# Kernel tuning notes

Hardware: AMD Instinct MI355X
Metric: run time of the kernel (lower is better)

## Reference

```python
import jax, jax.numpy as jnp
import numpy as np

B, T, C = 8, 1024, 512
H = 8
E = C // 2  # split_idx == per-head dim e


def setup_inputs() -> dict:
    key = jax.random.key(0)
    ks = jax.random.split(key, 6)
    s = 0.02
    return {
        "x": jax.random.normal(ks[0], (B, T, C), dtype=jnp.float32),
        "Wq": jax.random.normal(ks[1], (E * H, E), dtype=jnp.float32) * s,
        "Wk": jax.random.normal(ks[2], (E * H, E), dtype=jnp.float32) * s,
        "Wv": jax.random.normal(ks[3], (E * H, E), dtype=jnp.float32) * s,
        "Wu": jax.random.normal(ks[4], (C - E, E * H), dtype=jnp.float32) * s,
        "bu": jnp.zeros((C - E,), dtype=jnp.float32),
    }


def reference(x, Wq, Wk, Wv, Wu, bu):
    # coupling split: x1 drives attention, x2 gets additive update
    x1 = x[..., :E]           # [B,T,E]
    x2 = x[..., E:]           # [B,T,C-E]
    scale = E ** (-0.25)
    # torch Linear: y = x W^T ; output viewed as (heads, e) -> heads-major rows
    q = jnp.einsum('bti,oi->bto', x1, Wq).reshape(B, T, H, E) * scale
    k = jnp.einsum('bti,oi->bto', x1, Wk).reshape(B, T, H, E) * scale
    v = jnp.einsum('bti,oi->bto', x1, Wv).reshape(B, T, H, E)
    # attention scores [B,H,T,T]
    dot = jnp.einsum('bthe,bshe->bhts', q, k)
    attn = jax.nn.softmax(dot, axis=-1)
    out = jnp.einsum('bhts,bshe->bthe', attn, v).reshape(B, T, H * E)
    unified = jnp.einsum('bto,co->btc', out, Wu) + bu  # [B,T,C-E]
    return jnp.concatenate([x1, x2 + unified], axis=-1)
```

## Files before the change

kernel.cpp:

```cpp
#include <hip/hip_runtime.h>
#include <hip/hip_bf16.h>

#define BB 8
#define TT 1024
#define CC 512
#define HH 8
#define EE 256
#define MM (BB*TT)
#define HE (HH*EE)

using short8 = __attribute__((ext_vector_type(8))) short;
using f32x16 = __attribute__((ext_vector_type(16))) float;
using uint2v = __attribute__((ext_vector_type(2))) unsigned int;

__device__ __forceinline__ float bf2f(unsigned short u) {
  union { float f; unsigned int i; } v; v.i = ((unsigned int)u) << 16; return v.f;
}
__device__ __forceinline__ unsigned short f2bf(float f) {
  union { float f; unsigned int i; } v; v.f = f;
  unsigned int r = v.i + 0x7FFFu + ((v.i >> 16) & 1u);
  return (unsigned short)(r >> 16);
}
__device__ __forceinline__ unsigned int pk_bf16(float lo, float hi) {
  unsigned int r;
  asm("v_cvt_pk_bf16_f32 %0, %1, %2" : "=v"(r) : "v"(lo), "v"(hi));
  return r;
}
__device__ __forceinline__ void gll16(const void* g, void* l) {
  __builtin_amdgcn_global_load_lds(
      (const __attribute__((address_space(1))) unsigned int*)g,
      (__attribute__((address_space(3))) unsigned int*)l, 16, 0, 0);
}

#define FSTR 72
__global__ __launch_bounds__(512) void qkv_fused_kernel(const float* __restrict__ x,
                                                        const float* __restrict__ Wq,
                                                        const float* __restrict__ Wk,
                                                        const float* __restrict__ Wv,
                                                        unsigned short* __restrict__ outq,
                                                        unsigned short* __restrict__ outk,
                                                        unsigned short* __restrict__ outvt,
                                                        float* __restrict__ out) {
  __shared__ unsigned short smem[4 * 128 * FSTR];
  unsigned short* As = smem;
  unsigned short* Bs[3] = { smem + 128 * FSTR, smem + 2 * 128 * FSTR, smem + 3 * 128 * FSTR };

  const int tid = threadIdx.x;
  const int lane = tid & 63;
  const int wid = tid >> 6;
  const int wr = wid >> 2, wc = wid & 3;
  const int lo = lane & 31, hi = lane >> 5;

  int bid = blockIdx.x;
  int r = bid >> 3;
  int mt = (bid & 7) * 8 + (r & 7);
  int nt = r >> 3;
  const int m0 = mt * 128;
  const int n0 = nt * 128;

  const float* Wp[3] = { Wq, Wk, Wv };
  const float scl[3] = { 0.25f * 1.44269504089f, 0.25f, 1.0f };

  const int srow = tid >> 2;
  const int sc0 = (tid & 3) * 16;

  float4 ra[4], rb[3][4];
  f32x16 acc[3][2];
#pragma unroll
  for (int w = 0; w < 3; ++w)
#pragma unroll
    for (int mi = 0; mi < 2; ++mi)
#pragma unroll
      for (int q = 0; q < 16; ++q) acc[w][mi][q] = 0.f;

#pragma unroll
  for (int j = 0; j < 4; ++j)
    ra[j] = *reinterpret_cast<const float4*>(&x[(size_t)(m0 + srow) * CC + sc0 + 4 * j]);
#pragma unroll
  for (int w = 0; w < 3; ++w)
#pragma unroll
    for (int j = 0; j < 4; ++j)
      rb[w][j] = *reinterpret_cast<const float4*>(&Wp[w][(size_t)(n0 + srow) * EE + sc0 + 4 * j]);

  for (int t = 0; t < 4; ++t) {
    {
      union { unsigned int u[4]; short8 v; } p0, p1;
      p0.u[0] = pk_bf16(ra[0].x, ra[0].y); p0.u[1] = pk_bf16(ra[0].z, ra[0].w);
      p0.u[2] = pk_bf16(ra[1].x, ra[1].y); p0.u[3] = pk_bf16(ra[1].z, ra[1].w);
      p1.u[0] = pk_bf16(ra[2].x, ra[2].y); p1.u[1] = pk_bf16(ra[2].z, ra[2].w);
      p1.u[2] = pk_bf16(ra[3].x, ra[3].y); p1.u[3] = pk_bf16(ra[3].z, ra[3].w);
      *reinterpret_cast<short8*>(&As[srow * FSTR + sc0]) = p0.v;
      *reinterpret_cast<short8*>(&As[srow * FSTR + sc0 + 8]) = p1.v;
#pragma unroll
      for (int w = 0; w < 3; ++w) {
        union { unsigned int u[4]; short8 v; } q0, q1;
        q0.u[0] = pk_bf16(rb[w][0].x, rb[w][0].y); q0.u[1] = pk_bf16(rb[w][0].z, rb[w][0].w);
        q0.u[2] = pk_bf16(rb[w][1].x, rb[w][1].y); q0.u[3] = pk_bf16(rb[w][1].z, rb[w][1].w);
        q1.u[0] = pk_bf16(rb[w][2].x, rb[w][2].y); q1.u[1] = pk_bf16(rb[w][2].z, rb[w][2].w);
        q1.u[2] = pk_bf16(rb[w][3].x, rb[w][3].y); q1.u[3] = pk_bf16(rb[w][3].z, rb[w][3].w);
        *reinterpret_cast<short8*>(&Bs[w][srow * FSTR + sc0]) = q0.v;
        *reinterpret_cast<short8*>(&Bs[w][srow * FSTR + sc0 + 8]) = q1.v;
      }
    }
    if (n0 == 0) {
      int k0 = t * 64;
#pragma unroll
      for (int j = 0; j < 4; ++j)
        *reinterpret_cast<float4*>(&out[(size_t)(m0 + srow) * CC + k0 + sc0 + 4 * j]) = ra[j];
    }
    asm volatile("s_waitcnt lgkmcnt(0)" ::: "memory");
    __builtin_amdgcn_s_barrier();
    __builtin_amdgcn_sched_barrier(0);

    if (t + 1 < 4) {
      int k0 = (t + 1) * 64;
#pragma unroll
      for (int j = 0; j < 4; ++j)
        ra[j] = *reinterpret_cast<const float4*>(&x[(size_t)(m0 + srow) * CC + k0 + sc0 + 4 * j]);
#pragma unroll
      for (int w = 0; w < 3; ++w)
#pragma unroll
        for (int j = 0; j < 4; ++j)
          rb[w][j] = *reinterpret_cast<const float4*>(&Wp[w][(size_t)(n0 + srow) * EE + k0 + sc0 + 4 * j]);
    }

    __builtin_amdgcn_s_setprio(1);
#pragma unroll
    for (int ks = 0; ks < 4; ++ks) {
      short8 af[2];
#pragma unroll
      for (int mi = 0; mi < 2; ++mi)
        af[mi] = *reinterpret_cast<const short8*>(&As[(64 * wr + 32 * mi + lo) * FSTR + ks * 16 + hi * 8]);
#pragma unroll
      for (int w = 0; w < 3; ++w) {
        short8 bf = *reinterpret_cast<const short8*>(&Bs[w][(32 * wc + lo) * FSTR + ks * 16 + hi * 8]);
#pragma unroll
        for (int mi = 0; mi < 2; ++mi)
          acc[w][mi] = __builtin_amdgcn_mfma_f32_32x32x16_bf16(af[mi], bf, acc[w][mi], 0, 0, 0);
      }
    }
    __builtin_amdgcn_s_setprio(0);
    __builtin_amdgcn_s_barrier();
    __builtin_amdgcn_sched_barrier(0);
  }

#pragma unroll
  for (int w = 0; w < 2; ++w) {
    unsigned short* op = (w == 0) ? outq : outk;
#pragma unroll
    for (int mi = 0; mi < 2; ++mi) {
#pragma unroll
      for (int q = 0; q < 16; ++q) {
        int rr = (q & 3) + 8 * (q >> 2) + 4 * hi;
        int m = m0 + 64 * wr + 32 * mi + rr;
        int n = n0 + 32 * wc + lo;
        op[(size_t)m * HE + n] = f2bf(acc[w][mi][q] * scl[w]);
      }
    }
  }

  unsigned short* Tr = smem;
  __syncthreads();
#pragma unroll
  for (int mi = 0; mi < 2; ++mi)
#pragma unroll
    for (int q = 0; q < 16; ++q) {
      int rr = (q & 3) + 8 * (q >> 2) + 4 * hi;
      Tr[(32 * wc + lo) * 136 + 64 * wr + 32 * mi + rr] = f2bf(acc[2][mi][q]);
    }
  __syncthreads();
  {
    const int b = m0 >> 10;
    const int t0m = m0 & 1023;
#pragma unroll
    for (int p = 0; p < 4; ++p) {
      int nr = p * 32 + (tid >> 4);
      int chunk = tid & 15;
      int n = n0 + nr;
      size_t drow = ((size_t)b * 8 + (n >> 8)) * 256 + (n & 255);
      *reinterpret_cast<short8*>(&outvt[drow * TT + t0m + chunk * 8]) =
          *reinterpret_cast<const short8*>(&Tr[nr * 136 + chunk * 8]);
    }
  }
}

#define SBLK 32
__global__ __launch_bounds__(256, 2) void attn_kernel(const unsigned short* __restrict__ qg,
                                                      const unsigned short* __restrict__ kg,
                                                      const unsigned short* __restrict__ vtg,
                                                      unsigned short* __restrict__ og) {
  __shared__ char smem[66048];
  unsigned short* Kbuf = (unsigned short*)smem;
  unsigned short* Vbuf = (unsigned short*)(smem + 32768);
  float* lpart = (float*)(smem + 65536);

  const int tid = threadIdx.x;
  const int lane = tid & 63;
  const int wid = tid >> 6;
  const int lo = lane & 31, hi = lane >> 5;

  int logical = (blockIdx.x & 7) * 64 + (blockIdx.x >> 3);
  const int bh = logical >> 3;
  const int t0 = (logical & 7) * 128;
  const int b = bh >> 3, h = bh & 7;
  const size_t qkbase = (size_t)b * TT * HE + (size_t)h * EE;
  const size_t vtbase = (size_t)bh * EE * TT;
  const unsigned short* kg_base = kg + qkbase;
  const unsigned short* vt_base = vtg + vtbase;

  short8 qf[16];
  {
    const unsigned short* qrow = qg + qkbase + (size_t)(t0 + 32 * wid + lo) * HE + hi * 8;
#pragma unroll
    for (int ks = 0; ks < 16; ++ks)
      qf[ks] = *reinterpret_cast<const short8*>(qrow + ks * 16);
  }

  f32x16 Oacc[8];
#pragma unroll
  for (int et = 0; et < 8; ++et)
#pragma unroll
    for (int q = 0; q < 16; ++q) Oacc[et][q] = 0.f;
  float lacc = 0.f;

  const int k_sub = lane >> 5;
  const int k_g   = lane & 31;
  const int v_er  = lane >> 2;
  const int v_g   = lane & 3;
  const int v_gs  = v_g ^ ((lane >> 3) & 3);

#define STAGE_TILE(TIDX, BUF)                                                        \
  {                                                                                  \
    const unsigned short* kt = kg_base + (size_t)(TIDX) * SBLK * HE;                 \
    const unsigned short* vt = vt_base + (size_t)(TIDX) * SBLK;                      \
    unsigned short* Kb = Kbuf + (BUF) * (SBLK * 256);                                \
    unsigned short* Vb = Vbuf + (BUF) * (256 * SBLK);                                \
    _Pragma("unroll")                                                                \
    for (int i = 0; i < 4; ++i) {                                                    \
      int row = 8 * wid + 2 * i + k_sub;                                             \
      int gs = k_g ^ (row & 7);                                                      \
      gll16(kt + (size_t)row * HE + gs * 8, Kb + (8 * wid + 2 * i) * 256);           \
    }                                                                                \
    _Pragma("unroll")                                                                \
    for (int i = 0; i < 4; ++i) {                                                    \
      int row = 64 * wid + 16 * i + v_er;                                            \
      gll16(vt + (size_t)row * TT + v_gs * 8, Vb + (64 * wid + 16 * i) * SBLK);      \
    }                                                                                \
  }

  STAGE_TILE(0, 0)
  asm volatile("s_waitcnt vmcnt(0)" ::: "memory");
  __builtin_amdgcn_s_barrier();
  __builtin_amdgcn_sched_barrier(0);

  for (int t = 0; t < 32; ++t) {
    const int cur = t & 1;
    if (t + 1 < 32) STAGE_TILE(t + 1, cur ^ 1)

    const unsigned short* Kb = Kbuf + cur * (SBLK * 256);
    const unsigned short* Vb = Vbuf + cur * (256 * SBLK);

    f32x16 sacc;
#pragma unroll
    for (int q = 0; q < 16; ++q) sacc[q] = 0.f;
    const int sxor = lo & 7;
#pragma unroll
    for (int ks = 0; ks < 16; ++ks) {
      int slot = (ks * 2 + hi) ^ sxor;
      short8 kf = *reinterpret_cast<const short8*>(&Kb[lo * 256 + slot * 8]);
      sacc = __builtin_amdgcn_mfma_f32_32x32x16_bf16(kf, qf[ks], sacc, 0, 0, 0);
    }

    short8 pa[2];
#pragma unroll
    for (int ksl = 0; ksl < 2; ++ksl) {
      float p0 = __builtin_amdgcn_exp2f(sacc[8 * ksl + 0]);
      float p1 = __builtin_amdgcn_exp2f(sacc[8 * ksl + 1]);
      float p2 = __builtin_amdgcn_exp2f(sacc[8 * ksl + 2]);
      float p3 = __builtin_amdgcn_exp2f(sacc[8 * ksl + 3]);
      float p4 = __builtin_amdgcn_exp2f(sacc[8 * ksl + 4]);
      float p5 = __builtin_amdgcn_exp2f(sacc[8 * ksl + 5]);
      float p6 = __builtin_amdgcn_exp2f(sacc[8 * ksl + 6]);
      float p7 = __builtin_amdgcn_exp2f(sacc[8 * ksl + 7]);
      lacc += ((p0 + p1) + (p2 + p3)) + ((p4 + p5) + (p6 + p7));
      unsigned int a1 = pk_bf16(p0, p1), a2 = pk_bf16(p2, p3);
      unsigned int b1 = pk_bf16(p4, p5), b2 = pk_bf16(p6, p7);
      uint2v r1 = __builtin_amdgcn_permlane32_swap(a1, b1, false, false);
      uint2v r2 = __builtin_amdgcn_permlane32_swap(a2, b2, false, false);
      union { unsigned int u[4]; short8 v; } uu;
      uu.u[0] = r1[0]; uu.u[1] = r2[0]; uu.u[2] = r1[1]; uu.u[3] = r2[1];
      pa[ksl] = uu.v;
    }

    const int vxor = (lo >> 1) & 3;
#pragma unroll
    for (int et = 0; et < 8; ++et) {
      const int erow = et * 32 + lo;
#pragma unroll
      for (int ksl = 0; ksl < 2; ++ksl) {
        int slot = (2 * ksl + hi) ^ vxor;
        short8 vf = *reinterpret_cast<const short8*>(&Vb[erow * SBLK + slot * 8]);
        Oacc[et] = __builtin_amdgcn_mfma_f32_32x32x16_bf16(pa[ksl], vf, Oacc[et], 0, 0, 0);
      }
    }

    asm volatile("s_waitcnt vmcnt(0)" ::: "memory");
    __builtin_amdgcn_s_barrier();
    __builtin_amdgcn_sched_barrier(0);
  }

  lacc += __shfl_xor(lacc, 32);
  if (hi == 0) lpart[wid * 32 + lo] = lacc;
  __syncthreads();
#pragma unroll
  for (int q = 0; q < 16; ++q) {
    int rr = (q & 3) + 8 * (q >> 2) + 4 * hi;
    float inv = 1.0f / lpart[wid * 32 + rr];
    int tq = t0 + 32 * wid + rr;
#pragma unroll
    for (int et = 0; et < 8; ++et)
      og[qkbase + (size_t)tq * HE + et * 32 + lo] = f2bf(Oacc[et][q] * inv);
  }
#undef STAGE_TILE
}

#define PSTR 72
__global__ __launch_bounds__(256) void proj_mfma_kernel(const unsigned short* __restrict__ ao,
                                                        const float* __restrict__ Wu,
                                                        const float* __restrict__ bu,
                                                        const float* __restrict__ x,
                                                        float* __restrict__ out) {
  __shared__ unsigned short As[64 * PSTR];
  __shared__ unsigned short Bs[64 * PSTR];
  const int tid = threadIdx.x;
  const int lane = tid & 63;
  const int wid = tid >> 6;
  const int wr = wid >> 1, wc = wid & 1;
  const int lo = lane & 31, hi = lane >> 5;

  int bid = blockIdx.x;
  int r = bid >> 3;
  int mt = (bid & 7) * 16 + (r & 15);
  int nt = r >> 4;
  const int m0 = mt * 64;
  const int n0 = nt * 64;

  const int arow = tid >> 2;
  const int ag0 = (tid & 3) * 2;
  const int brow = tid >> 2;
  const int bg0 = (tid & 3) * 4;

  short8 raA[2];
  float4 raB[4];
  f32x16 acc;
#pragma unroll
  for (int q = 0; q < 16; ++q) acc[q] = 0.f;

#pragma unroll
  for (int j = 0; j < 2; ++j)
    raA[j] = *reinterpret_cast<const short8*>(&ao[(size_t)(m0 + arow) * HE + (ag0 + j) * 8]);
#pragma unroll
  for (int g = 0; g < 4; ++g)
    raB[g] = *reinterpret_cast<const float4*>(&Wu[(size_t)(n0 + brow) * HE + (bg0 + g) * 4]);

  for (int t = 0; t < 32; ++t) {
#pragma unroll
    for (int j = 0; j < 2; ++j)
      *reinterpret_cast<short8*>(&As[arow * PSTR + (ag0 + j) * 8]) = raA[j];
    {
      union { unsigned int u[4]; short8 v; } w0, w1;
      w0.u[0] = pk_bf16(raB[0].x, raB[0].y); w0.u[1] = pk_bf16(raB[0].z, raB[0].w);
      w0.u[2] = pk_bf16(raB[1].x, raB[1].y); w0.u[3] = pk_bf16(raB[1].z, raB[1].w);
      w1.u[0] = pk_bf16(raB[2].x, raB[2].y); w1.u[1] = pk_bf16(raB[2].z, raB[2].w);
      w1.u[2] = pk_bf16(raB[3].x, raB[3].y); w1.u[3] = pk_bf16(raB[3].z, raB[3].w);
      *reinterpret_cast<short8*>(&Bs[brow * PSTR + ag0 * 8]) = w0.v;
      *reinterpret_cast<short8*>(&Bs[brow * PSTR + (ag0 + 1) * 8]) = w1.v;
    }
    asm volatile("s_waitcnt lgkmcnt(0)" ::: "memory");
    __builtin_amdgcn_s_barrier();
    __builtin_amdgcn_sched_barrier(0);

    if (t + 1 < 32) {
      int k0 = (t + 1) * 64;
#pragma unroll
      for (int j = 0; j < 2; ++j)
        raA[j] = *reinterpret_cast<const short8*>(&ao[(size_t)(m0 + arow) * HE + k0 + (ag0 + j) * 8]);
#pragma unroll
      for (int g = 0; g < 4; ++g)
        raB[g] = *reinterpret_cast<const float4*>(&Wu[(size_t)(n0 + brow) * HE + k0 + (bg0 + g) * 4]);
    }

    __builtin_amdgcn_s_setprio(1);
#pragma unroll
    for (int ks = 0; ks < 4; ++ks) {
      short8 af = *reinterpret_cast<const short8*>(&As[(32 * wr + lo) * PSTR + ks * 16 + hi * 8]);
      short8 bf = *reinterpret_cast<const short8*>(&Bs[(32 * wc + lo) * PSTR + ks * 16 + hi * 8]);
      acc = __builtin_amdgcn_mfma_f32_32x32x16_bf16(af, bf, acc, 0, 0, 0);
    }
    __builtin_amdgcn_s_setprio(0);
    __builtin_amdgcn_s_barrier();
    __builtin_amdgcn_sched_barrier(0);
  }

  {
    int n = n0 + 32 * wc + lo;
    float bias = bu[n];
#pragma unroll
    for (int q = 0; q < 16; ++q) {
      int rr = (q & 3) + 8 * (q >> 2) + 4 * hi;
      int m = m0 + 32 * wr + rr;
      float o = acc[q] + x[(size_t)m * CC + EE + n] + bias;
      out[(size_t)m * CC + EE + n] = o;
    }
  }
}

extern "C" void kernel_launch(void* const* d_in, const int* in_sizes, int n_in,
                              void* d_out, int out_size, void* d_ws, size_t ws_size,
                              hipStream_t stream) {
  const float* x  = (const float*)d_in[0];
  const float* Wq = (const float*)d_in[1];
  const float* Wk = (const float*)d_in[2];
  const float* Wv = (const float*)d_in[3];
  const float* Wu = (const float*)d_in[4];
  const float* bu = (const float*)d_in[5];
  float* out = (float*)d_out;

  unsigned short* q  = (unsigned short*)d_ws;
  unsigned short* k  = q + (size_t)MM * HE;
  unsigned short* vt = k + (size_t)MM * HE;
  unsigned short* ao = vt + (size_t)MM * HE;

  qkv_fused_kernel<<<dim3(1024), dim3(512), 0, stream>>>(x, Wq, Wk, Wv, q, k, vt, out);

  attn_kernel<<<dim3(512), dim3(256), 0, stream>>>(q, k, vt, ao);

  proj_mfma_kernel<<<dim3(512), dim3(256), 0, stream>>>(ao, Wu, bu, x, out);
}
```

Baseline: 164.8 us.

## Pre-convert x and weights to bf16 in fragment layout before QKV GEMM

Adds a prep kernel that converts x to bf16 and copies x into the output. It also packs Wq/Wk/Wv, with the Q/K scales folded in, into a bf16 layout that matches the MFMA B-fragment order. The QKV kernel then loads the whole 64x256 A tile into LDS once via global_load_lds with XOR swizzle and streams B fragments directly from global memory with no K-loop barriers. This removes repeated fp32-to-bf16 conversion and LDS staging of weights, but adds an extra launch and an extra round trip through memory for x. It also reuses the ao workspace as scratch for xb and the packed weights.

```diff
diff --git a/kernel.cpp b/kernel.cpp
--- a/kernel.cpp
+++ b/kernel.cpp
@@ -13,9 +13,6 @@
 using f32x16 = __attribute__((ext_vector_type(16))) float;
 using uint2v = __attribute__((ext_vector_type(2))) unsigned int;
 
-__device__ __forceinline__ float bf2f(unsigned short u) {
-  union { float f; unsigned int i; } v; v.i = ((unsigned int)u) << 16; return v.f;
-}
 __device__ __forceinline__ unsigned short f2bf(float f) {
   union { float f; unsigned int i; } v; v.f = f;
   unsigned int r = v.i + 0x7FFFu + ((v.i >> 16) & 1u);
@@ -32,39 +29,78 @@
       (__attribute__((address_space(3))) unsigned int*)l, 16, 0, 0);
 }
 
-#define FSTR 72
-__global__ __launch_bounds__(512) void qkv_fused_kernel(const float* __restrict__ x,
-                                                        const float* __restrict__ Wq,
-                                                        const float* __restrict__ Wk,
-                                                        const float* __restrict__ Wv,
-                                                        unsigned short* __restrict__ outq,
-                                                        unsigned short* __restrict__ outk,
-                                                        unsigned short* __restrict__ outvt,
-                                                        float* __restrict__ out) {
-  __shared__ unsigned short smem[4 * 128 * FSTR];
-  unsigned short* As = smem;
-  unsigned short* Bs[3] = { smem + 128 * FSTR, smem + 2 * 128 * FSTR, smem + 3 * 128 * FSTR };
+__global__ __launch_bounds__(256) void prep_kernel(const float* __restrict__ x,
+                                                   const float* __restrict__ Wq,
+                                                   const float* __restrict__ Wk,
+                                                   const float* __restrict__ Wv,
+                                                   unsigned short* __restrict__ xb,
+                                                   unsigned short* __restrict__ wf,
+                                                   float* __restrict__ out) {
+  int t = blockIdx.x * 256 + threadIdx.x;
+  if (t < 262144) {
+    int m = t >> 5;
+    int c8 = (t & 31) * 8;
+    float4 a = *reinterpret_cast<const float4*>(&x[(size_t)m * CC + c8]);
+    float4 b = *reinterpret_cast<const float4*>(&x[(size_t)m * CC + c8 + 4]);
+    union { unsigned int u[4]; short8 v; } o;
+    o.u[0] = pk_bf16(a.x, a.y); o.u[1] = pk_bf16(a.z, a.w);
+    o.u[2] = pk_bf16(b.x, b.y); o.u[3] = pk_bf16(b.z, b.w);
+    *reinterpret_cast<short8*>(&xb[(size_t)m * 256 + c8]) = o.v;
+    *reinterpret_cast<float4*>(&out[(size_t)m * CC + c8]) = a;
+    *reinterpret_cast<float4*>(&out[(size_t)m * CC + c8 + 4]) = b;
+  } else {
+    int t2 = t - 262144;
+    int lane = t2 & 63;
+    int rest = t2 >> 6;
+    int ks = rest & 15;
+    int ng = (rest >> 4) & 63;
+    int w = rest >> 10;
+    const float* Wp = (w == 0) ? Wq : (w == 1) ? Wk : Wv;
+    const float scl = (w == 0) ? 0.25f * 1.44269504089f : (w == 1) ? 0.25f : 1.0f;
+    int n = ng * 32 + (lane & 31);
+    int e0 = ks * 16 + (lane >> 5) * 8;
+    float4 a = *reinterpret_cast<const float4*>(&Wp[(size_t)n * EE + e0]);
+    float4 b = *reinterpret_cast<const float4*>(&Wp[(size_t)n * EE + e0 + 4]);
+    union { unsigned int u[4]; short8 v; } o;
+    o.u[0] = pk_bf16(a.x * scl, a.y * scl); o.u[1] = pk_bf16(a.z * scl, a.w * scl);
+    o.u[2] = pk_bf16(b.x * scl, b.y * scl); o.u[3] = pk_bf16(b.z * scl, b.w * scl);
+    *reinterpret_cast<short8*>(&wf[(size_t)t2 * 8]) = o.v;
+  }
+}
+
+__global__ __launch_bounds__(256) void qkv_static_kernel(const unsigned short* __restrict__ xb,
+                                                         const unsigned short* __restrict__ wf,
+                                                         unsigned short* __restrict__ outq,
+                                                         unsigned short* __restrict__ outk,
+                                                         unsigned short* __restrict__ outvt) {
+  __shared__ unsigned short Ab[64 * 256];
 
   const int tid = threadIdx.x;
   const int lane = tid & 63;
   const int wid = tid >> 6;
-  const int wr = wid >> 2, wc = wid & 3;
+  const int wc = wid;
   const int lo = lane & 31, hi = lane >> 5;
 
   int bid = blockIdx.x;
   int r = bid >> 3;
-  int mt = (bid & 7) * 8 + (r & 7);
-  int nt = r >> 3;
-  const int m0 = mt * 128;
+  int mt = (bid & 7) * 16 + (r & 15);
+  int nt = r >> 4;
+  const int m0 = mt * 64;
   const int n0 = nt * 128;
 
-  const float* Wp[3] = { Wq, Wk, Wv };
-  const float scl[3] = { 0.25f * 1.44269504089f, 0.25f, 1.0f };
-
-  const int srow = tid >> 2;
-  const int sc0 = (tid & 3) * 16;
-
-  float4 ra[4], rb[3][4];
+  {
+    const int a_sub = lane >> 5;
+    const int a_g = lane & 31;
+#pragma unroll
+    for (int i = 0; i < 8; ++i) {
+      int row = 16 * wid + 2 * i + a_sub;
+      int gs = a_g ^ (row & 7);
+      gll16(xb + (size_t)(m0 + row) * 256 + gs * 8, Ab + (16 * wid + 2 * i) * 256);
+    }
+  }
+  asm volatile("s_waitcnt vmcnt(0)" ::: "memory");
+  __builtin_amdgcn_s_barrier();
+
   f32x16 acc[3][2];
 #pragma unroll
   for (int w = 0; w < 3; ++w)
@@ -73,75 +109,28 @@
 #pragma unroll
       for (int q = 0; q < 16; ++q) acc[w][mi][q] = 0.f;
 
-#pragma unroll
-  for (int j = 0; j < 4; ++j)
-    ra[j] = *reinterpret_cast<const float4*>(&x[(size_t)(m0 + srow) * CC + sc0 + 4 * j]);
-#pragma unroll
-  for (int w = 0; w < 3; ++w)
-#pragma unroll
-    for (int j = 0; j < 4; ++j)
-      rb[w][j] = *reinterpret_cast<const float4*>(&Wp[w][(size_t)(n0 + srow) * EE + sc0 + 4 * j]);
-
-  for (int t = 0; t < 4; ++t) {
-    {
-      union { unsigned int u[4]; short8 v; } p0, p1;
-      p0.u[0] = pk_bf16(ra[0].x, ra[0].y); p0.u[1] = pk_bf16(ra[0].z, ra[0].w);
-      p0.u[2] = pk_bf16(ra[1].x, ra[1].y); p0.u[3] = pk_bf16(ra[1].z, ra[1].w);
-      p1.u[0] = pk_bf16(ra[2].x, ra[2].y); p1.u[1] = pk_bf16(ra[2].z, ra[2].w);
-      p1.u[2] = pk_bf16(ra[3].x, ra[3].y); p1.u[3] = pk_bf16(ra[3].z, ra[3].w);
-      *reinterpret_cast<short8*>(&As[srow * FSTR + sc0]) = p0.v;
-      *reinterpret_cast<short8*>(&As[srow * FSTR + sc0 + 8]) = p1.v;
-#pragma unroll
-      for (int w = 0; w < 3; ++w) {
-        union { unsigned int u[4]; short8 v; } q0, q1;
-        q0.u[0] = pk_bf16(rb[w][0].x, rb[w][0].y); q0.u[1] = pk_bf16(rb[w][0].z, rb[w][0].w);
-        q0.u[2] = pk_bf16(rb[w][1].x, rb[w][1].y); q0.u[3] = pk_bf16(rb[w][1].z, rb[w][1].w);
-        q1.u[0] = pk_bf16(rb[w][2].x, rb[w][2].y); q1.u[1] = pk_bf16(rb[w][2].z, rb[w][2].w);
-        q1.u[2] = pk_bf16(rb[w][3].x, rb[w][3].y); q1.u[3] = pk_bf16(rb[w][3].z, rb[w][3].w);
-        *reinterpret_cast<short8*>(&Bs[w][srow * FSTR + sc0]) = q0.v;
-        *reinterpret_cast<short8*>(&Bs[w][srow * FSTR + sc0 + 8]) = q1.v;
-      }
-    }
-    if (n0 == 0) {
-      int k0 = t * 64;
-#pragma unroll
-      for (int j = 0; j < 4; ++j)
-        *reinterpret_cast<float4*>(&out[(size_t)(m0 + srow) * CC + k0 + sc0 + 4 * j]) = ra[j];
-    }
-    asm volatile("s_waitcnt lgkmcnt(0)" ::: "memory");
-    __builtin_amdgcn_s_barrier();
-    __builtin_amdgcn_sched_barrier(0);
-
-    if (t + 1 < 4) {
-      int k0 = (t + 1) * 64;
-#pragma unroll
-      for (int j = 0; j < 4; ++j)
-        ra[j] = *reinterpret_cast<const float4*>(&x[(size_t)(m0 + srow) * CC + k0 + sc0 + 4 * j]);
-#pragma unroll
-      for (int w = 0; w < 3; ++w)
-#pragma unroll
-        for (int j = 0; j < 4; ++j)
-          rb[w][j] = *reinterpret_cast<const float4*>(&Wp[w][(size_t)(n0 + srow) * EE + k0 + sc0 + 4 * j]);
-    }
-
-    __builtin_amdgcn_s_setprio(1);
-#pragma unroll
-    for (int ks = 0; ks < 4; ++ks) {
-      short8 af[2];
+  const int ng = nt * 4 + wc;
+  const short8* wfp = reinterpret_cast<const short8*>(wf);
+  const int sxor = lo & 7;
+
+#pragma unroll
+  for (int ks = 0; ks < 16; ++ks) {
+    short8 bf[3];
+#pragma unroll
+    for (int w = 0; w < 3; ++w)
+      bf[w] = wfp[(size_t)((w * 64 + ng) * 16 + ks) * 64 + lane];
+    short8 af[2];
+#pragma unroll
+    for (int mi = 0; mi < 2; ++mi) {
+      int row = 32 * mi + lo;
+      int slot = (ks * 2 + hi) ^ sxor;
+      af[mi] = *reinterpret_cast<const short8*>(&Ab[row * 256 + slot * 8]);
+    }
+#pragma unroll
+    for (int w = 0; w < 3; ++w)
 #pragma unroll
       for (int mi = 0; mi < 2; ++mi)
-        af[mi] = *reinterpret_cast<const short8*>(&As[(64 * wr + 32 * mi + lo) * FSTR + ks * 16 + hi * 8]);
-#pragma unroll
-      for (int w = 0; w < 3; ++w) {
-        short8 bf = *reinterpret_cast<const short8*>(&Bs[w][(32 * wc + lo) * FSTR + ks * 16 + hi * 8]);
-#pragma unroll
-        for (int mi = 0; mi < 2; ++mi)
-          acc[w][mi] = __builtin_amdgcn_mfma_f32_32x32x16_bf16(af[mi], bf, acc[w][mi], 0, 0, 0);
-      }
-    }
-    __builtin_amdgcn_s_setprio(0);
-    __builtin_amdgcn_s_barrier();
-    __builtin_amdgcn_sched_barrier(0);
+        acc[w][mi] = __builtin_amdgcn_mfma_f32_32x32x16_bf16(af[mi], bf[w], acc[w][mi], 0, 0, 0);
   }
 
 #pragma unroll
@@ -152,21 +141,21 @@
 #pragma unroll
       for (int q = 0; q < 16; ++q) {
         int rr = (q & 3) + 8 * (q >> 2) + 4 * hi;
-        int m = m0 + 64 * wr + 32 * mi + rr;
+        int m = m0 + 32 * mi + rr;
         int n = n0 + 32 * wc + lo;
-        op[(size_t)m * HE + n] = f2bf(acc[w][mi][q] * scl[w]);
+        op[(size_t)m * HE + n] = f2bf(acc[w][mi][q]);
       }
     }
   }
 
-  unsigned short* Tr = smem;
+  unsigned short* Tr = Ab;
   __syncthreads();
 #pragma unroll
   for (int mi = 0; mi < 2; ++mi)
 #pragma unroll
     for (int q = 0; q < 16; ++q) {
       int rr = (q & 3) + 8 * (q >> 2) + 4 * hi;
-      Tr[(32 * wc + lo) * 136 + 64 * wr + 32 * mi + rr] = f2bf(acc[2][mi][q]);
+      Tr[(32 * wc + lo) * 72 + 32 * mi + rr] = f2bf(acc[2][mi][q]);
     }
   __syncthreads();
   {
@@ -174,12 +163,12 @@
     const int t0m = m0 & 1023;
 #pragma unroll
     for (int p = 0; p < 4; ++p) {
-      int nr = p * 32 + (tid >> 4);
-      int chunk = tid & 15;
+      int nr = p * 32 + (tid >> 3);
+      int chunk = tid & 7;
       int n = n0 + nr;
       size_t drow = ((size_t)b * 8 + (n >> 8)) * 256 + (n & 255);
       *reinterpret_cast<short8*>(&outvt[drow * TT + t0m + chunk * 8]) =
-          *reinterpret_cast<const short8*>(&Tr[nr * 136 + chunk * 8]);
+          *reinterpret_cast<const short8*>(&Tr[nr * 72 + chunk * 8]);
     }
   }
 }
@@ -430,8 +419,12 @@
   unsigned short* k  = q + (size_t)MM * HE;
   unsigned short* vt = k + (size_t)MM * HE;
   unsigned short* ao = vt + (size_t)MM * HE;
-
-  qkv_fused_kernel<<<dim3(1024), dim3(512), 0, stream>>>(x, Wq, Wk, Wv, q, k, vt, out);
+  unsigned short* xb = ao;
+  unsigned short* wfb = xb + (size_t)MM * EE;
+
+  prep_kernel<<<dim3(1792), dim3(256), 0, stream>>>(x, Wq, Wk, Wv, xb, wfb, out);
+
+  qkv_static_kernel<<<dim3(2048), dim3(256), 0, stream>>>(xb, wfb, q, k, vt);
 
   attn_kernel<<<dim3(512), dim3(256), 0, stream>>>(q, k, vt, ao);
 
```

New measurement: 154.5 us. 1.07x faster.
